# Kernel optimization log

Hardware: AMD Instinct MI355X
Metric: run time of the kernel (lower is better)

## Reference

```python
import jax, jax.numpy as jnp
import numpy as np

HEADS = 16
DIM_HEAD = 64
EPS = 1e-12  # F.normalize default eps


def setup_inputs() -> dict:
    key = jax.random.key(0)
    k1, k2, k3 = jax.random.split(key, 3)
    b, n, dim = 2, 2048, 1024
    dim_inner = HEADS * DIM_HEAD
    x = jax.random.normal(k1, (b, n, dim), dtype=jnp.float32)
    gamma = jnp.ones((dim,), dtype=jnp.float32)
    w_qkv = jax.random.normal(k2, (dim, 3 * dim_inner), dtype=jnp.float32) * 0.02
    w_out = jax.random.normal(k3, (dim_inner, dim), dtype=jnp.float32) * 0.02
    return {"x": x, "gamma": gamma, "w_qkv": w_qkv, "w_out": w_out}


def reference(x, gamma, w_qkv, w_out):
    b, n, dim = x.shape
    h, d = HEADS, DIM_HEAD
    scale = d ** -0.5

    # RMSNorm (lucidrains): F.normalize(x, dim=-1) * dim**0.5 * gamma
    norm = jnp.sqrt(jnp.sum(x * x, axis=-1, keepdims=True))
    xn = x / jnp.maximum(norm, EPS) * (dim ** 0.5) * gamma

    # qkv projection -> [b, n, 3, h, d] -> q/k/v each [b, h, n, d]
    qkv = (xn @ w_qkv).reshape(b, n, 3, h, d)
    qkv = jnp.transpose(qkv, (2, 0, 3, 1, 4))
    q, k, v = qkv[0], qkv[1], qkv[2]

    q = q * scale
    sim = jnp.einsum('bhid,bhjd->bhij', q, k)  # [b, h, n, n]
    causal_mask = jnp.triu(jnp.ones((n, n), dtype=bool), k=1)
    mask_value = -jnp.finfo(sim.dtype).max
    sim = jnp.where(causal_mask, mask_value, sim)
    attn = jax.nn.softmax(sim, axis=-1)
    out = jnp.einsum('bhij,bhjd->bhid', attn, v)  # [b, h, n, d]

    out = jnp.transpose(out, (0, 2, 1, 3)).reshape(b, n, h * d)
    return out @ w_out
```

## Files before the change

kernel.cpp:

```cpp
#include <hip/hip_runtime.h>

typedef __attribute__((ext_vector_type(8))) short bf16x8;
typedef __attribute__((ext_vector_type(4))) short bf16x4;
typedef __attribute__((ext_vector_type(4))) float f32x4;

static __device__ __forceinline__ short f2bf(float f) {
    union { float f; unsigned u; } v; v.f = f;
    unsigned r = v.u + 0x7fffu + ((v.u >> 16) & 1u);
    return (short)(r >> 16);
}

static __device__ __forceinline__ float exp2_fast(float x) {
    float r; asm("v_exp_f32 %0, %1" : "=v"(r) : "v"(x)); return r;
}

static __device__ __forceinline__ void async_copy16(const short* g, short* l) {
    __builtin_amdgcn_global_load_lds((const __attribute__((address_space(1))) void*)g,
                                     (__attribute__((address_space(3))) void*)l,
                                     16, 0, 0);
}

#define BARX()                                            \
    do {                                                  \
        asm volatile("" ::: "memory");                    \
        __builtin_amdgcn_s_barrier();                     \
        __builtin_amdgcn_sched_barrier(0);                \
    } while (0)

#define HEADS 16
#define DHEAD 64
#define NSEQ  2048
#define DIM   1024
#define BATCH 2
#define ROWS  (BATCH * NSEQ)
#define NQKV  (3 * HEADS * DHEAD)

#define QSCALE 0.18033688f

__global__ __launch_bounds__(256) void prep_kernel(const float* __restrict__ x,
                                                   const float* __restrict__ gamma,
                                                   const float* __restrict__ w_qkv,
                                                   const float* __restrict__ w_out,
                                                   short* __restrict__ xn,
                                                   short* __restrict__ wqkvT,
                                                   short* __restrict__ woutT) {
    const int blk = blockIdx.x;
    const int t = threadIdx.x;
    __shared__ float tile[64][65];
    __shared__ float part[4];

    if (blk < 1024) {
        const float* in;  short* out;  int C, bx, by;
        if (blk < 768) { in = w_qkv; out = wqkvT; C = NQKV; bx = blk % 48; by = blk / 48; }
        else           { in = w_out; out = woutT; C = DIM;  bx = (blk - 768) & 15; by = (blk - 768) >> 4; }
        const int gx = bx * 64, gy = by * 64;
        const int lc4 = (t & 15) * 4;
        const int lr  = t >> 4;
#pragma unroll
        for (int p = 0; p < 4; ++p) {
            const float4 v = *(const float4*)&in[(size_t)(gy + p * 16 + lr) * C + gx + lc4];
            tile[p * 16 + lr][lc4 + 0] = v.x;
            tile[p * 16 + lr][lc4 + 1] = v.y;
            tile[p * 16 + lr][lc4 + 2] = v.z;
            tile[p * 16 + lr][lc4 + 3] = v.w;
        }
        __syncthreads();
        const int oc  = t >> 2;
        const int or4 = (t & 3) * 16;
#pragma unroll
        for (int j = 0; j < 4; ++j) {
            bf16x4 w;
#pragma unroll
            for (int r = 0; r < 4; ++r) w[r] = f2bf(tile[or4 + j * 4 + r][oc]);
            *(bf16x4*)&out[(size_t)(gx + oc) * DIM + gy + or4 + j * 4] = w;
        }
    } else {
        const int row = blk - 1024;
        const float4 v = ((const float4*)(x + (size_t)row * DIM))[t];
        float s = v.x * v.x + v.y * v.y + v.z * v.z + v.w * v.w;
#pragma unroll
        for (int off = 32; off > 0; off >>= 1) s += __shfl_down(s, off, 64);
        if ((t & 63) == 0) part[t >> 6] = s;
        __syncthreads();
        const float tot = part[0] + part[1] + part[2] + part[3];
        const float scale = 32.0f / fmaxf(sqrtf(tot), 1e-12f);
        const float4 g = ((const float4*)gamma)[t];
        bf16x4 o;
        o[0] = f2bf(v.x * scale * g.x);
        o[1] = f2bf(v.y * scale * g.y);
        o[2] = f2bf(v.z * scale * g.z);
        o[3] = f2bf(v.w * scale * g.w);
        *(bf16x4*)(xn + (size_t)row * DIM + t * 4) = o;
    }
}

__global__ __launch_bounds__(512, 2) void gemm_qkv(const short* __restrict__ A,
                                                   const short* __restrict__ Bt,
                                                   short* __restrict__ qkOut,
                                                   short* __restrict__ vtOut) {
    __shared__ alignas(16) short lA[2][256 * 64];
    __shared__ alignas(16) short lB[2][192 * 64];
    const int tid = threadIdx.x;
    const int lane = tid & 63, wid = tid >> 6;
    const int quad = lane >> 4, l16 = lane & 15;
    const int wm = wid >> 2, wn = wid & 3;

    int flat = blockIdx.x;
    flat = (flat & 7) * 32 + (flat >> 3);
    const int mb = (flat >> 4) * 256;
    const int nb = (flat & 15) * 192;

    f32x4 acc[8][3];
#pragma unroll
    for (int i = 0; i < 8; ++i)
#pragma unroll
        for (int j = 0; j < 3; ++j) acc[i][j] = (f32x4){0.f, 0.f, 0.f, 0.f};

    const int srow = tid >> 3;
    const int scol = (tid & 7) * 8;
    const int scolx = scol ^ ((srow & 7) * 8);

    auto stageA = [&](int kb, int buf) {
#pragma unroll
        for (int c = 0; c < 4; ++c) {
            const int row = c * 64 + srow;
            async_copy16(&A[(size_t)(mb + row) * 1024 + kb + scolx],
                         &lA[buf][row * 64 + scol]);
        }
    };
    auto stageB = [&](int kb, int buf) {
#pragma unroll
        for (int c = 0; c < 3; ++c) {
            const int row = c * 64 + srow;
            async_copy16(&Bt[(size_t)(nb + row) * 1024 + kb + scolx],
                         &lB[buf][row * 64 + scol]);
        }
    };
    auto rdA = [&](int buf, int mt, int kh) -> bf16x8 {
        const int row = wm * 128 + mt * 16 + l16;
        const int col = (kh * 32 + quad * 8) ^ ((row & 7) * 8);
        return *(const bf16x8*)&lA[buf][row * 64 + col];
    };
    auto rdB = [&](int buf, int nt, int kh) -> bf16x8 {
        const int row = wn * 48 + nt * 16 + l16;
        const int col = (kh * 32 + quad * 8) ^ ((row & 7) * 8);
        return *(const bf16x8*)&lB[buf][row * 64 + col];
    };

    stageA(0, 0);
    stageB(0, 0);
    asm volatile("s_waitcnt vmcnt(0)" ::: "memory");
    BARX();

    int cur = 0;
    for (int kt = 0; kt < 16; ++kt) {
        bf16x8 a[4][2], b01[2][2], b2[2];
#pragma unroll
        for (int mt = 0; mt < 4; ++mt)
#pragma unroll
            for (int kh = 0; kh < 2; ++kh) a[mt][kh] = rdA(cur, mt, kh);
#pragma unroll
        for (int nt = 0; nt < 2; ++nt)
#pragma unroll
            for (int kh = 0; kh < 2; ++kh) b01[nt][kh] = rdB(cur, nt, kh);
        if (kt < 15) {
            stageA((kt + 1) * 64, cur ^ 1);
            stageB((kt + 1) * 64, cur ^ 1);
        }
        BARX();
        __builtin_amdgcn_s_setprio(1);
#pragma unroll
        for (int kh = 0; kh < 2; ++kh)
#pragma unroll
            for (int mt = 0; mt < 4; ++mt)
#pragma unroll
                for (int nt = 0; nt < 2; ++nt)
                    acc[mt][nt] = __builtin_amdgcn_mfma_f32_16x16x32_bf16(
                        a[mt][kh], b01[nt][kh], acc[mt][nt], 0, 0, 0);
        __builtin_amdgcn_s_setprio(0);
#pragma unroll
        for (int kh = 0; kh < 2; ++kh) b2[kh] = rdB(cur, 2, kh);
        BARX();
        __builtin_amdgcn_s_setprio(1);
#pragma unroll
        for (int kh = 0; kh < 2; ++kh)
#pragma unroll
            for (int mt = 0; mt < 4; ++mt)
                acc[mt][2] = __builtin_amdgcn_mfma_f32_16x16x32_bf16(
                    a[mt][kh], b2[kh], acc[mt][2], 0, 0, 0);
        __builtin_amdgcn_s_setprio(0);
#pragma unroll
        for (int mt = 0; mt < 4; ++mt)
#pragma unroll
            for (int kh = 0; kh < 2; ++kh) a[mt][kh] = rdA(cur, mt + 4, kh);
        BARX();
        __builtin_amdgcn_s_setprio(1);
#pragma unroll
        for (int kh = 0; kh < 2; ++kh)
#pragma unroll
            for (int mt = 0; mt < 4; ++mt)
                acc[mt + 4][2] = __builtin_amdgcn_mfma_f32_16x16x32_bf16(
                    a[mt][kh], b2[kh], acc[mt + 4][2], 0, 0, 0);
        __builtin_amdgcn_s_setprio(0);
        asm volatile("s_waitcnt vmcnt(0)" ::: "memory");
        BARX();
        __builtin_amdgcn_s_setprio(1);
#pragma unroll
        for (int kh = 0; kh < 2; ++kh)
#pragma unroll
            for (int mt = 0; mt < 4; ++mt)
#pragma unroll
                for (int nt = 0; nt < 2; ++nt)
                    acc[mt + 4][nt] = __builtin_amdgcn_mfma_f32_16x16x32_bf16(
                        a[mt][kh], b01[nt][kh], acc[mt + 4][nt], 0, 0, 0);
        __builtin_amdgcn_s_setprio(0);
        cur ^= 1;
    }

#pragma unroll
    for (int mt = 0; mt < 8; ++mt) {
#pragma unroll
        for (int nt = 0; nt < 3; ++nt) {
            const int grow0 = mb + wm * 128 + mt * 16 + quad * 4;
            const int gcol  = nb + wn * 48 + nt * 16 + l16;
            const int s3 = gcol >> 10, rem = gcol & 1023;
            const int hh = rem >> 6, dd = rem & 63;
            const int bb = grow0 >> 11, npos0 = grow0 & 2047;
            if (s3 == 2) {
                bf16x4 vw;
#pragma unroll
                for (int r = 0; r < 4; ++r) vw[r] = f2bf(acc[mt][nt][r]);
                *(bf16x4*)&vtOut[((size_t)(bb * 16 + hh) * 64 + dd) * 2048 + npos0] = vw;
            } else {
                const float sc = (s3 == 0) ? QSCALE : 1.0f;
#pragma unroll
                for (int r = 0; r < 4; ++r)
                    qkOut[(size_t)((s3 * 32 + bb * 16 + hh) * 2048 + npos0 + r) * 64 + dd] =
                        f2bf(acc[mt][nt][r] * sc);
            }
        }
    }
}

template <int MT, int NT, int WM, int WN>
__global__ __launch_bounds__(256) void gemm_out(const short* __restrict__ A,
                                                const short* __restrict__ Bt,
                                                float* __restrict__ Cout,
                                                int K, int N) {
    constexpr int TM = WM * MT * 16;
    constexpr int TN = WN * NT * 16;
    __shared__ alignas(16) short lds_a[2][TM * 32];
    __shared__ alignas(16) short lds_b[2][TN * 32];
    const int tid = threadIdx.x;
    const int lane = tid & 63, wid = tid >> 6;
    const int quad = lane >> 4, l16 = lane & 15;
    const int wm = wid / WN, wn = wid % WN;

    const int nx = gridDim.x;
    const int nwg = nx * gridDim.y;
    int flat = blockIdx.y * nx + blockIdx.x;
    if ((nwg & 7) == 0) {
        const int q8 = nwg >> 3;
        flat = (flat & 7) * q8 + (flat >> 3);
    }
    const int mb = (flat / nx) * TM, nb = (flat % nx) * TN;

    f32x4 acc[MT][NT];
#pragma unroll
    for (int i = 0; i < MT; ++i)
#pragma unroll
        for (int j = 0; j < NT; ++j) acc[i][j] = (f32x4){0.f, 0.f, 0.f, 0.f};

    const int lr = lane >> 2;
    const int lc = (lane & 3) * 8;

    auto stage = [&](int kb, int buf) {
#pragma unroll
        for (int c = 0; c < TM / 64; ++c) {
            const int row = c * 64 + wid * 16 + lr;
            async_copy16(&A[(size_t)(mb + row) * K + kb + lc], &lds_a[buf][row * 32 + lc]);
        }
#pragma unroll
        for (int c = 0; c < TN / 64; ++c) {
            const int row = c * 64 + wid * 16 + lr;
            async_copy16(&Bt[(size_t)(nb + row) * K + kb + lc], &lds_b[buf][row * 32 + lc]);
        }
    };

    stage(0, 0);
    __syncthreads();

    int cur = 0;
    for (int kb = 0; kb < K; kb += 32) {
        if (kb + 32 < K) stage(kb + 32, cur ^ 1);

        bf16x8 af[MT], bfr[NT];
#pragma unroll
        for (int mt = 0; mt < MT; ++mt)
            af[mt] = *(const bf16x8*)&lds_a[cur][(wm * MT * 16 + mt * 16 + l16) * 32 + quad * 8];
#pragma unroll
        for (int nt = 0; nt < NT; ++nt)
            bfr[nt] = *(const bf16x8*)&lds_b[cur][(wn * NT * 16 + nt * 16 + l16) * 32 + quad * 8];
#pragma unroll
        for (int mt = 0; mt < MT; ++mt)
#pragma unroll
            for (int nt = 0; nt < NT; ++nt)
                acc[mt][nt] = __builtin_amdgcn_mfma_f32_16x16x32_bf16(af[mt], bfr[nt],
                                                                      acc[mt][nt], 0, 0, 0);
        __syncthreads();
        cur ^= 1;
    }

#pragma unroll
    for (int mt = 0; mt < MT; ++mt) {
#pragma unroll
        for (int nt = 0; nt < NT; ++nt) {
            const int grow0 = mb + wm * MT * 16 + mt * 16 + quad * 4;
            const int gcol  = nb + wn * NT * 16 + nt * 16 + l16;
#pragma unroll
            for (int r = 0; r < 4; ++r)
                Cout[(size_t)(grow0 + r) * N + gcol] = acc[mt][nt][r];
        }
    }
}

__global__ __launch_bounds__(256, 3) void attn_kernel(const short* __restrict__ qg,
                                                      const short* __restrict__ kg,
                                                      const short* __restrict__ vtg,
                                                      short* __restrict__ og) {
    const int tid = threadIdx.x;
    const int wid = tid >> 6, lane = tid & 63;
    const int quad = lane >> 4, l16 = lane & 15;
    const int blk = blockIdx.x;
    const int qt = (blk < 256) ? (15 - (blk >> 5)) : ((blk - 256) >> 5);
    const int bh = blk & 31;
    const size_t base = (size_t)bh * (NSEQ * DHEAD);
    const int bb = bh >> 4, hh = bh & 15;
    const int qbase = qt * 128 + wid * 32;
    const int ntiles = 2 * qt + 2;

    __shared__ alignas(16) short kT[2][4096];
    __shared__ alignas(16) short vT[2][4096];

    const int r0 = tid >> 3;
    const int slot = tid & 7;
    auto stage = [&](int t, short* KT_, short* VT_) {
        const int kb = t * 64;
#pragma unroll
        for (int c = 0; c < 2; ++c) {
            const int r = c * 32 + r0;
            const int ss = ((slot ^ (r & 7)) * 8);
            async_copy16(&kg[base + (size_t)(kb + r) * 64 + ss], &KT_[r * 64 + slot * 8]);
            async_copy16(&vtg[base + (size_t)r * 2048 + kb + ss], &VT_[r * 64 + slot * 8]);
        }
    };

    bf16x8 qf[2][2];
#pragma unroll
    for (int qn = 0; qn < 2; ++qn)
#pragma unroll
        for (int kh = 0; kh < 2; ++kh)
            qf[qn][kh] = *(const bf16x8*)&qg[base + (size_t)(qbase + qn * 16 + l16) * DHEAD +
                                            kh * 32 + quad * 8];

    float li[2] = {0.f, 0.f};
    f32x4 accO[2][4];
#pragma unroll
    for (int qn = 0; qn < 2; ++qn)
#pragma unroll
        for (int nc = 0; nc < 4; ++nc) accO[qn][nc] = (f32x4){0.f, 0.f, 0.f, 0.f};

    const int swz = (l16 & 7) * 8;

    auto tile_step = [&](const short* KT_, const short* VT_, int t) {
        const int kb = t * 64;
        f32x4 sf[2][4];
#pragma unroll
        for (int m = 0; m < 4; ++m) {
            const int rb = (m * 16 + l16) * 64;
            const bf16x8 kf0 = *(const bf16x8*)&KT_[rb + ((quad * 8) ^ swz)];
            const bf16x8 kf1 = *(const bf16x8*)&KT_[rb + ((32 + quad * 8) ^ swz)];
#pragma unroll
            for (int qn = 0; qn < 2; ++qn) {
                f32x4 z = (f32x4){0.f, 0.f, 0.f, 0.f};
                z = __builtin_amdgcn_mfma_f32_16x16x32_bf16(kf0, qf[qn][0], z, 0, 0, 0);
                sf[qn][m] = __builtin_amdgcn_mfma_f32_16x16x32_bf16(kf1, qf[qn][1], z, 0, 0, 0);
            }
        }
        if (kb + 64 > qbase) {
#pragma unroll
            for (int qn = 0; qn < 2; ++qn) {
                const int myq = qbase + qn * 16 + l16;
#pragma unroll
                for (int m = 0; m < 4; ++m)
#pragma unroll
                    for (int r = 0; r < 4; ++r)
                        if (kb + m * 16 + quad * 4 + r > myq) sf[qn][m][r] = -3.0e38f;
            }
        }
        unsigned c0[2][4], c1[2][4];
#pragma unroll
        for (int qn = 0; qn < 2; ++qn) {
            float rs = 0.f;
#pragma unroll
            for (int m = 0; m < 4; ++m) {
                const float p0 = exp2_fast(sf[qn][m][0]);
                const float p1 = exp2_fast(sf[qn][m][1]);
                const float p2 = exp2_fast(sf[qn][m][2]);
                const float p3 = exp2_fast(sf[qn][m][3]);
                rs += (p0 + p1) + (p2 + p3);
                asm("v_cvt_pk_bf16_f32 %0, %1, %2" : "=v"(c0[qn][m]) : "v"(p0), "v"(p1));
                asm("v_cvt_pk_bf16_f32 %0, %1, %2" : "=v"(c1[qn][m]) : "v"(p2), "v"(p3));
            }
            li[qn] += rs;
        }
        bf16x8 pf[2][2];
#pragma unroll
        for (int qn = 0; qn < 2; ++qn)
#pragma unroll
            for (int ks = 0; ks < 2; ++ks) {
                unsigned a0 = c0[qn][2 * ks], b0 = c0[qn][2 * ks + 1];
                unsigned a1 = c1[qn][2 * ks], b1 = c1[qn][2 * ks + 1];
                asm("v_permlane32_swap_b32 %0, %1" : "+v"(a0), "+v"(b0));
                asm("v_permlane16_swap_b32 %0, %1" : "+v"(a0), "+v"(b0));
                asm("v_permlane32_swap_b32 %0, %1" : "+v"(a1), "+v"(b1));
                asm("v_permlane16_swap_b32 %0, %1" : "+v"(a1), "+v"(b1));
                union { bf16x8 v; unsigned u[4]; } t8;
                t8.u[0] = a0; t8.u[1] = a1; t8.u[2] = b0; t8.u[3] = b1;
                pf[qn][ks] = t8.v;
            }
#pragma unroll
        for (int nc = 0; nc < 4; ++nc) {
            const int rb = (nc * 16 + l16) * 64;
            const bf16x8 vf0 = *(const bf16x8*)&VT_[rb + ((quad * 8) ^ swz)];
            const bf16x8 vf1 = *(const bf16x8*)&VT_[rb + ((32 + quad * 8) ^ swz)];
#pragma unroll
            for (int qn = 0; qn < 2; ++qn) {
                accO[qn][nc] = __builtin_amdgcn_mfma_f32_16x16x32_bf16(vf0, pf[qn][0],
                                                                      accO[qn][nc], 0, 0, 0);
                accO[qn][nc] = __builtin_amdgcn_mfma_f32_16x16x32_bf16(vf1, pf[qn][1],
                                                                      accO[qn][nc], 0, 0, 0);
            }
        }
    };

    stage(0, kT[0], vT[0]);
    __syncthreads();
    for (int t = 0; t < ntiles; t += 2) {
        stage(t + 1, kT[1], vT[1]);
        tile_step(kT[0], vT[0], t);
        __syncthreads();
        if (t + 2 < ntiles) stage(t + 2, kT[0], vT[0]);
        tile_step(kT[1], vT[1], t + 1);
        __syncthreads();
    }

#pragma unroll
    for (int qn = 0; qn < 2; ++qn) {
        li[qn] += __shfl_xor(li[qn], 16, 64);
        li[qn] += __shfl_xor(li[qn], 32, 64);
        const float inv = 1.0f / li[qn];
        const int npos = qbase + qn * 16 + l16;
#pragma unroll
        for (int nc = 0; nc < 4; ++nc) {
            bf16x4 ow;
#pragma unroll
            for (int r = 0; r < 4; ++r) ow[r] = f2bf(accO[qn][nc][r] * inv);
            *(bf16x4*)&og[(size_t)(bb * 2048 + npos) * 1024 + hh * 64 + nc * 16 + quad * 4] = ow;
        }
    }
}

extern "C" void kernel_launch(void* const* d_in, const int* in_sizes, int n_in,
                              void* d_out, int out_size, void* d_ws, size_t ws_size,
                              hipStream_t stream) {
    const float* x     = (const float*)d_in[0];
    const float* gamma = (const float*)d_in[1];
    const float* w_qkv = (const float*)d_in[2];
    const float* w_out = (const float*)d_in[3];
    float* out = (float*)d_out;
    char* ws = (char*)d_ws;

    short* xn     = (short*)(ws);
    short* wqkvT  = (short*)(ws + 8388608);
    short* woutT  = (short*)(ws + 14680064);
    short* q      = (short*)(ws + 16777216);
    short* k      = q + 32 * 2048 * 64;
    short* vt     = k + 32 * 2048 * 64;
    short* attn   = (short*)(ws + 41943040);

    prep_kernel<<<5120, 256, 0, stream>>>(x, gamma, w_qkv, w_out, xn, wqkvT, woutT);
    gemm_qkv<<<256, 512, 0, stream>>>(xn, wqkvT, q, vt);
    attn_kernel<<<512, 256, 0, stream>>>(q, k, vt, attn);
    gemm_out<2, 4, 4, 1><<<dim3(DIM / 64, ROWS / 128), 256, 0, stream>>>(attn, woutT, out,
                                                                         DIM, DIM);
}
```

Measured before the change: 166.9 us.

## Double K-step depth in attention and output GEMM with swizzled LDS tiles

The attention kernel now stages 128-key K/V tiles per step instead of 64, which halves the number of barriers and async-copy rounds per query tile. The V-tile LDS swizzle is widened to 16 slots, and occupancy drops to 2 blocks per CU. The output GEMM is specialized to fixed sizes with a 64-wide K step, XOR-swizzled LDS layout and a hardcoded grid remap, reducing loop iterations and LDS bank conflicts. The cost is more LDS per block, which lowers occupancy in exchange for fewer sync points.

```diff
diff --git a/kernel.cpp b/kernel.cpp
--- a/kernel.cpp
+++ b/kernel.cpp
@@ -242,48 +242,40 @@
     }
 }
 
-template <int MT, int NT, int WM, int WN>
-__global__ __launch_bounds__(256) void gemm_out(const short* __restrict__ A,
-                                                const short* __restrict__ Bt,
-                                                float* __restrict__ Cout,
-                                                int K, int N) {
-    constexpr int TM = WM * MT * 16;
-    constexpr int TN = WN * NT * 16;
-    __shared__ alignas(16) short lds_a[2][TM * 32];
-    __shared__ alignas(16) short lds_b[2][TN * 32];
+__global__ __launch_bounds__(256, 3) void gemm_out(const short* __restrict__ A,
+                                                   const short* __restrict__ Bt,
+                                                   float* __restrict__ Cout) {
+    __shared__ alignas(16) short lA2[2][128 * 64];
+    __shared__ alignas(16) short lB2[2][64 * 64];
     const int tid = threadIdx.x;
     const int lane = tid & 63, wid = tid >> 6;
     const int quad = lane >> 4, l16 = lane & 15;
-    const int wm = wid / WN, wn = wid % WN;
-
-    const int nx = gridDim.x;
-    const int nwg = nx * gridDim.y;
+
+    const int nx = 16;
     int flat = blockIdx.y * nx + blockIdx.x;
-    if ((nwg & 7) == 0) {
-        const int q8 = nwg >> 3;
-        flat = (flat & 7) * q8 + (flat >> 3);
-    }
-    const int mb = (flat / nx) * TM, nb = (flat % nx) * TN;
-
-    f32x4 acc[MT][NT];
-#pragma unroll
-    for (int i = 0; i < MT; ++i)
-#pragma unroll
-        for (int j = 0; j < NT; ++j) acc[i][j] = (f32x4){0.f, 0.f, 0.f, 0.f};
-
-    const int lr = lane >> 2;
-    const int lc = (lane & 3) * 8;
+    flat = (flat & 7) * 64 + (flat >> 3);
+    const int mb = (flat / nx) * 128, nb = (flat % nx) * 64;
+
+    f32x4 acc[2][4];
+#pragma unroll
+    for (int i = 0; i < 2; ++i)
+#pragma unroll
+        for (int j = 0; j < 4; ++j) acc[i][j] = (f32x4){0.f, 0.f, 0.f, 0.f};
 
     auto stage = [&](int kb, int buf) {
 #pragma unroll
-        for (int c = 0; c < TM / 64; ++c) {
-            const int row = c * 64 + wid * 16 + lr;
-            async_copy16(&A[(size_t)(mb + row) * K + kb + lc], &lds_a[buf][row * 32 + lc]);
-        }
-#pragma unroll
-        for (int c = 0; c < TN / 64; ++c) {
-            const int row = c * 64 + wid * 16 + lr;
-            async_copy16(&Bt[(size_t)(nb + row) * K + kb + lc], &lds_b[buf][row * 32 + lc]);
+        for (int p = 0; p < 4; ++p) {
+            const int ck = p * 256 + tid;
+            const int ar = ck >> 3, as_ = ck & 7;
+            async_copy16(&A[(size_t)(mb + ar) * 1024 + kb + ((as_ ^ (ar & 7)) * 8)],
+                         &lA2[buf][ck * 8]);
+        }
+#pragma unroll
+        for (int p = 0; p < 2; ++p) {
+            const int cb = p * 256 + tid;
+            const int br = cb >> 3, bs = cb & 7;
+            async_copy16(&Bt[(size_t)(nb + br) * 1024 + kb + ((bs ^ (br & 7)) * 8)],
+                         &lB2[buf][cb * 8]);
         }
     };
 
@@ -291,40 +283,52 @@
     __syncthreads();
 
     int cur = 0;
-    for (int kb = 0; kb < K; kb += 32) {
-        if (kb + 32 < K) stage(kb + 32, cur ^ 1);
-
-        bf16x8 af[MT], bfr[NT];
-#pragma unroll
-        for (int mt = 0; mt < MT; ++mt)
-            af[mt] = *(const bf16x8*)&lds_a[cur][(wm * MT * 16 + mt * 16 + l16) * 32 + quad * 8];
-#pragma unroll
-        for (int nt = 0; nt < NT; ++nt)
-            bfr[nt] = *(const bf16x8*)&lds_b[cur][(wn * NT * 16 + nt * 16 + l16) * 32 + quad * 8];
-#pragma unroll
-        for (int mt = 0; mt < MT; ++mt)
-#pragma unroll
-            for (int nt = 0; nt < NT; ++nt)
-                acc[mt][nt] = __builtin_amdgcn_mfma_f32_16x16x32_bf16(af[mt], bfr[nt],
-                                                                      acc[mt][nt], 0, 0, 0);
+    for (int kt = 0; kt < 16; ++kt) {
+        if (kt + 1 < 16) stage((kt + 1) * 64, cur ^ 1);
+
+        bf16x8 af[2][2], bfr[4][2];
+#pragma unroll
+        for (int mt = 0; mt < 2; ++mt) {
+            const int row = wid * 32 + mt * 16 + l16;
+#pragma unroll
+            for (int kh = 0; kh < 2; ++kh)
+                af[mt][kh] = *(const bf16x8*)&lA2[cur][row * 64 +
+                                                      (((kh * 4 + quad) ^ (row & 7)) * 8)];
+        }
+#pragma unroll
+        for (int nt = 0; nt < 4; ++nt) {
+            const int row = nt * 16 + l16;
+#pragma unroll
+            for (int kh = 0; kh < 2; ++kh)
+                bfr[nt][kh] = *(const bf16x8*)&lB2[cur][row * 64 +
+                                                       (((kh * 4 + quad) ^ (row & 7)) * 8)];
+        }
+#pragma unroll
+        for (int kh = 0; kh < 2; ++kh)
+#pragma unroll
+            for (int mt = 0; mt < 2; ++mt)
+#pragma unroll
+                for (int nt = 0; nt < 4; ++nt)
+                    acc[mt][nt] = __builtin_amdgcn_mfma_f32_16x16x32_bf16(
+                        af[mt][kh], bfr[nt][kh], acc[mt][nt], 0, 0, 0);
         __syncthreads();
         cur ^= 1;
     }
 
 #pragma unroll
-    for (int mt = 0; mt < MT; ++mt) {
-#pragma unroll
-        for (int nt = 0; nt < NT; ++nt) {
-            const int grow0 = mb + wm * MT * 16 + mt * 16 + quad * 4;
-            const int gcol  = nb + wn * NT * 16 + nt * 16 + l16;
+    for (int mt = 0; mt < 2; ++mt) {
+#pragma unroll
+        for (int nt = 0; nt < 4; ++nt) {
+            const int grow0 = mb + wid * 32 + mt * 16 + quad * 4;
+            const int gcol  = nb + nt * 16 + l16;
 #pragma unroll
             for (int r = 0; r < 4; ++r)
-                Cout[(size_t)(grow0 + r) * N + gcol] = acc[mt][nt][r];
-        }
-    }
-}
-
-__global__ __launch_bounds__(256, 3) void attn_kernel(const short* __restrict__ qg,
+                Cout[(size_t)(grow0 + r) * DIM + gcol] = acc[mt][nt][r];
+        }
+    }
+}
+
+__global__ __launch_bounds__(256, 2) void attn_kernel(const short* __restrict__ qg,
                                                       const short* __restrict__ kg,
                                                       const short* __restrict__ vtg,
                                                       short* __restrict__ og) {
@@ -337,21 +341,26 @@
     const size_t base = (size_t)bh * (NSEQ * DHEAD);
     const int bb = bh >> 4, hh = bh & 15;
     const int qbase = qt * 128 + wid * 32;
-    const int ntiles = 2 * qt + 2;
-
-    __shared__ alignas(16) short kT[2][4096];
-    __shared__ alignas(16) short vT[2][4096];
-
-    const int r0 = tid >> 3;
-    const int slot = tid & 7;
-    auto stage = [&](int t, short* KT_, short* VT_) {
-        const int kb = t * 64;
-#pragma unroll
-        for (int c = 0; c < 2; ++c) {
-            const int r = c * 32 + r0;
-            const int ss = ((slot ^ (r & 7)) * 8);
-            async_copy16(&kg[base + (size_t)(kb + r) * 64 + ss], &KT_[r * 64 + slot * 8]);
-            async_copy16(&vtg[base + (size_t)r * 2048 + kb + ss], &VT_[r * 64 + slot * 8]);
+    const int steps = qt + 1;
+
+    __shared__ alignas(16) short kT[2][128 * 64];
+    __shared__ alignas(16) short vT[2][64 * 128];
+
+    auto stage = [&](int s, int buf) {
+        const int kb = s * 128;
+#pragma unroll
+        for (int p = 0; p < 4; ++p) {
+            const int ck = p * 256 + tid;
+            const int kr = ck >> 3, ksl = ck & 7;
+            async_copy16(&kg[base + (size_t)(kb + kr) * 64 + ((ksl ^ (kr & 7)) * 8)],
+                         &kT[buf][ck * 8]);
+        }
+#pragma unroll
+        for (int p = 0; p < 4; ++p) {
+            const int cv = p * 256 + tid;
+            const int vr = cv >> 4, vsl = cv & 15;
+            async_copy16(&vtg[base + (size_t)vr * 2048 + kb + ((vsl ^ (vr & 15)) * 8)],
+                         &vT[buf][cv * 8]);
         }
     };
 
@@ -370,89 +379,95 @@
 #pragma unroll
         for (int nc = 0; nc < 4; ++nc) accO[qn][nc] = (f32x4){0.f, 0.f, 0.f, 0.f};
 
-    const int swz = (l16 & 7) * 8;
-
-    auto tile_step = [&](const short* KT_, const short* VT_, int t) {
-        const int kb = t * 64;
-        f32x4 sf[2][4];
-#pragma unroll
-        for (int m = 0; m < 4; ++m) {
-            const int rb = (m * 16 + l16) * 64;
-            const bf16x8 kf0 = *(const bf16x8*)&KT_[rb + ((quad * 8) ^ swz)];
-            const bf16x8 kf1 = *(const bf16x8*)&KT_[rb + ((32 + quad * 8) ^ swz)];
+    auto tile_step = [&](int buf, int s) {
+        const int kb = s * 128;
+        bf16x8 pf[2][4];
+#pragma unroll
+        for (int h = 0; h < 2; ++h) {
+            f32x4 sf[2][4];
+#pragma unroll
+            for (int m = 0; m < 4; ++m) {
+                const int row = h * 64 + m * 16 + l16;
+                const int rb = row * 64;
+                const int sw = (row & 7) * 8;
+                const bf16x8 kf0 = *(const bf16x8*)&kT[buf][rb + ((quad * 8) ^ sw)];
+                const bf16x8 kf1 = *(const bf16x8*)&kT[buf][rb + ((32 + quad * 8) ^ sw)];
+#pragma unroll
+                for (int qn = 0; qn < 2; ++qn) {
+                    f32x4 z = (f32x4){0.f, 0.f, 0.f, 0.f};
+                    z = __builtin_amdgcn_mfma_f32_16x16x32_bf16(kf0, qf[qn][0], z, 0, 0, 0);
+                    sf[qn][m] = __builtin_amdgcn_mfma_f32_16x16x32_bf16(kf1, qf[qn][1], z,
+                                                                        0, 0, 0);
+                }
+            }
+            if (kb + h * 64 + 64 > qbase) {
+#pragma unroll
+                for (int qn = 0; qn < 2; ++qn) {
+                    const int myq = qbase + qn * 16 + l16;
+#pragma unroll
+                    for (int m = 0; m < 4; ++m)
+#pragma unroll
+                        for (int r = 0; r < 4; ++r)
+                            if (kb + h * 64 + m * 16 + quad * 4 + r > myq)
+                                sf[qn][m][r] = -3.0e38f;
+                }
+            }
+            unsigned c0[2][4], c1[2][4];
 #pragma unroll
             for (int qn = 0; qn < 2; ++qn) {
-                f32x4 z = (f32x4){0.f, 0.f, 0.f, 0.f};
-                z = __builtin_amdgcn_mfma_f32_16x16x32_bf16(kf0, qf[qn][0], z, 0, 0, 0);
-                sf[qn][m] = __builtin_amdgcn_mfma_f32_16x16x32_bf16(kf1, qf[qn][1], z, 0, 0, 0);
+                float rs = 0.f;
+#pragma unroll
+                for (int m = 0; m < 4; ++m) {
+                    const float p0 = exp2_fast(sf[qn][m][0]);
+                    const float p1 = exp2_fast(sf[qn][m][1]);
+                    const float p2 = exp2_fast(sf[qn][m][2]);
+                    const float p3 = exp2_fast(sf[qn][m][3]);
+                    rs += (p0 + p1) + (p2 + p3);
+                    asm("v_cvt_pk_bf16_f32 %0, %1, %2" : "=v"(c0[qn][m]) : "v"(p0), "v"(p1));
+                    asm("v_cvt_pk_bf16_f32 %0, %1, %2" : "=v"(c1[qn][m]) : "v"(p2), "v"(p3));
+                }
+                li[qn] += rs;
             }
-        }
-        if (kb + 64 > qbase) {
-#pragma unroll
-            for (int qn = 0; qn < 2; ++qn) {
-                const int myq = qbase + qn * 16 + l16;
-#pragma unroll
-                for (int m = 0; m < 4; ++m)
-#pragma unroll
-                    for (int r = 0; r < 4; ++r)
-                        if (kb + m * 16 + quad * 4 + r > myq) sf[qn][m][r] = -3.0e38f;
+#pragma unroll
+            for (int qn = 0; qn < 2; ++qn)
+#pragma unroll
+                for (int ks = 0; ks < 2; ++ks) {
+                    unsigned a0 = c0[qn][2 * ks], b0 = c0[qn][2 * ks + 1];
+                    unsigned a1 = c1[qn][2 * ks], b1 = c1[qn][2 * ks + 1];
+                    asm("v_permlane32_swap_b32 %0, %1" : "+v"(a0), "+v"(b0));
+                    asm("v_permlane16_swap_b32 %0, %1" : "+v"(a0), "+v"(b0));
+                    asm("v_permlane32_swap_b32 %0, %1" : "+v"(a1), "+v"(b1));
+                    asm("v_permlane16_swap_b32 %0, %1" : "+v"(a1), "+v"(b1));
+                    union { bf16x8 v; unsigned u[4]; } t8;
+                    t8.u[0] = a0; t8.u[1] = a1; t8.u[2] = b0; t8.u[3] = b1;
+                    pf[qn][h * 2 + ks] = t8.v;
+                }
+        }
+#pragma unroll
+        for (int nc = 0; nc < 4; ++nc) {
+            const int row = nc * 16 + l16;
+            const int rb = row * 128;
+#pragma unroll
+            for (int ks = 0; ks < 4; ++ks) {
+                const bf16x8 vf =
+                    *(const bf16x8*)&vT[buf][rb + (((ks * 4 + quad) ^ (row & 15)) * 8)];
+#pragma unroll
+                for (int qn = 0; qn < 2; ++qn)
+                    accO[qn][nc] = __builtin_amdgcn_mfma_f32_16x16x32_bf16(vf, pf[qn][ks],
+                                                                          accO[qn][nc],
+                                                                          0, 0, 0);
             }
         }
-        unsigned c0[2][4], c1[2][4];
-#pragma unroll
-        for (int qn = 0; qn < 2; ++qn) {
-            float rs = 0.f;
-#pragma unroll
-            for (int m = 0; m < 4; ++m) {
-                const float p0 = exp2_fast(sf[qn][m][0]);
-                const float p1 = exp2_fast(sf[qn][m][1]);
-                const float p2 = exp2_fast(sf[qn][m][2]);
-                const float p3 = exp2_fast(sf[qn][m][3]);
-                rs += (p0 + p1) + (p2 + p3);
-                asm("v_cvt_pk_bf16_f32 %0, %1, %2" : "=v"(c0[qn][m]) : "v"(p0), "v"(p1));
-                asm("v_cvt_pk_bf16_f32 %0, %1, %2" : "=v"(c1[qn][m]) : "v"(p2), "v"(p3));
-            }
-            li[qn] += rs;
-        }
-        bf16x8 pf[2][2];
-#pragma unroll
-        for (int qn = 0; qn < 2; ++qn)
-#pragma unroll
-            for (int ks = 0; ks < 2; ++ks) {
-                unsigned a0 = c0[qn][2 * ks], b0 = c0[qn][2 * ks + 1];
-                unsigned a1 = c1[qn][2 * ks], b1 = c1[qn][2 * ks + 1];
-                asm("v_permlane32_swap_b32 %0, %1" : "+v"(a0), "+v"(b0));
-                asm("v_permlane16_swap_b32 %0, %1" : "+v"(a0), "+v"(b0));
-                asm("v_permlane32_swap_b32 %0, %1" : "+v"(a1), "+v"(b1));
-                asm("v_permlane16_swap_b32 %0, %1" : "+v"(a1), "+v"(b1));
-                union { bf16x8 v; unsigned u[4]; } t8;
-                t8.u[0] = a0; t8.u[1] = a1; t8.u[2] = b0; t8.u[3] = b1;
-                pf[qn][ks] = t8.v;
-            }
-#pragma unroll
-        for (int nc = 0; nc < 4; ++nc) {
-            const int rb = (nc * 16 + l16) * 64;
-            const bf16x8 vf0 = *(const bf16x8*)&VT_[rb + ((quad * 8) ^ swz)];
-            const bf16x8 vf1 = *(const bf16x8*)&VT_[rb + ((32 + quad * 8) ^ swz)];
-#pragma unroll
-            for (int qn = 0; qn < 2; ++qn) {
-                accO[qn][nc] = __builtin_amdgcn_mfma_f32_16x16x32_bf16(vf0, pf[qn][0],
-                                                                      accO[qn][nc], 0, 0, 0);
-                accO[qn][nc] = __builtin_amdgcn_mfma_f32_16x16x32_bf16(vf1, pf[qn][1],
-                                                                      accO[qn][nc], 0, 0, 0);
-            }
-        }
-    };
-
-    stage(0, kT[0], vT[0]);
+    };
+
+    stage(0, 0);
     __syncthreads();
-    for (int t = 0; t < ntiles; t += 2) {
-        stage(t + 1, kT[1], vT[1]);
-        tile_step(kT[0], vT[0], t);
+    int cur = 0;
+    for (int s = 0; s < steps; ++s) {
+        if (s + 1 < steps) stage(s + 1, cur ^ 1);
+        tile_step(cur, s);
         __syncthreads();
-        if (t + 2 < ntiles) stage(t + 2, kT[0], vT[0]);
-        tile_step(kT[1], vT[1], t + 1);
-        __syncthreads();
+        cur ^= 1;
     }
 
 #pragma unroll
@@ -492,6 +507,5 @@
     prep_kernel<<<5120, 256, 0, stream>>>(x, gamma, w_qkv, w_out, xn, wqkvT, woutT);
     gemm_qkv<<<256, 512, 0, stream>>>(xn, wqkvT, q, vt);
     attn_kernel<<<512, 256, 0, stream>>>(q, k, vt, attn);
-    gemm_out<2, 4, 4, 1><<<dim3(DIM / 64, ROWS / 128), 256, 0, stream>>>(attn, woutT, out,
-                                                                         DIM, DIM);
-}
+    gemm_out<<<dim3(16, 32), 256, 0, stream>>>(attn, woutT, out);
+}
```

After: 162.4 us. -2.7%, faster.
